# Performance work log

Measured on AMD Instinct MI355X. Metric: run time of the kernel, lower is better.

## Reference

```python
import jax, jax.numpy as jnp
from jax import lax
import numpy as np

DIM = 384
HEADS = 8
SR = 2
B, D0, D1, D2 = 4, 16, 16, 16
N = 1 + D0 * D1 * D2


def setup_inputs() -> dict:
    key = jax.random.key(0)
    ks = jax.random.split(key, 8)
    s = 0.02
    return {
        "x": jax.random.normal(ks[0], (B, N, DIM), dtype=jnp.float32),
        "q_w": jax.random.normal(ks[1], (DIM, DIM), dtype=jnp.float32) * s,
        "kv_w": jax.random.normal(ks[2], (2 * DIM, DIM), dtype=jnp.float32) * s,
        "proj_w": jax.random.normal(ks[3], (DIM, DIM), dtype=jnp.float32) * s,
        "proj_b": jnp.zeros((DIM,), dtype=jnp.float32),
        "sr_w": jax.random.normal(ks[4], (DIM, 1, SR, SR, SR), dtype=jnp.float32) * s,  # depthwise (groups=dim)
        "sr_b": jnp.zeros((DIM,), dtype=jnp.float32),
        "ln_g": jnp.ones((DIM,), dtype=jnp.float32),
        "ln_b": jnp.zeros((DIM,), dtype=jnp.float32),
        "d0": D0, "d1": D1, "d2": D2,
    }


def reference(x, q_w, kv_w, proj_w, proj_b, sr_w, sr_b, ln_g, ln_b, d0, d1, d2):
    B_, N_, C = x.shape
    hd = C // HEADS
    scale = hd ** -0.5

    # q projection -> [B, H, N, hd]
    q = (x @ q_w.T).reshape(B_, N_, HEADS, hd).transpose(0, 2, 1, 3)

    # spatial reduction of patch tokens (keep CLS token)
    x_ = x[:, 1:].transpose(0, 2, 1).reshape(B_, C, d0, d1, d2)
    x_ = lax.conv_general_dilated(
        x_, sr_w, window_strides=(SR, SR, SR), padding="VALID",
        dimension_numbers=("NCDHW", "OIDHW", "NCDHW"), feature_group_count=C,
    ) + sr_b[None, :, None, None, None]
    x_ = x_.reshape(B_, C, -1).transpose(0, 2, 1)           # [B, M-1, C]
    x_ = jnp.concatenate([x[:, 0:1], x_], axis=1)            # [B, M, C]

    # LayerNorm (eps=1e-5)
    mu = jnp.mean(x_, axis=-1, keepdims=True)
    var = jnp.var(x_, axis=-1, keepdims=True)
    x_ = (x_ - mu) / jnp.sqrt(var + 1e-5) * ln_g + ln_b

    M = x_.shape[1]
    kv = (x_ @ kv_w.T).reshape(B_, M, 2, HEADS, hd).transpose(2, 0, 3, 1, 4)
    k, v = kv[0], kv[1]                                      # [B, H, M, hd]

    attn = jax.nn.softmax(jnp.einsum("bhnd,bhmd->bhnm", q, k) * scale, axis=-1)
    out = jnp.einsum("bhnm,bhmd->bhnd", attn, v)
    out = out.transpose(0, 2, 1, 3).reshape(B_, N_, C)
    return out @ proj_w.T + proj_b
```

## Files before the change

kernel.cpp:

```cpp
#include <hip/hip_runtime.h>

typedef unsigned short u16;
typedef unsigned int u32;
typedef __bf16 bf16x8 __attribute__((ext_vector_type(8)));
typedef float f32x4 __attribute__((ext_vector_type(4)));

#define NTOK 4097
#define MTOK 513
#define MPAD 544
#define KPAD 640
#define NPAD_Q 4224
#define ROWS_X 16512

__device__ __forceinline__ u16 f2bf(float f) {
  u32 u = __builtin_bit_cast(u32, f);
  u = u + 0x7FFFu + ((u >> 16) & 1u);
  return (u16)(u >> 16);
}
__device__ __forceinline__ u16 f2bf_fast(float f) {
  u32 u = __builtin_bit_cast(u32, f);
  return (u16)((u + 0x8000u) >> 16);
}

__device__ __forceinline__ float fexp2(float x) {
#if __has_builtin(__builtin_amdgcn_exp2f)
  return __builtin_amdgcn_exp2f(x);
#else
  float r;
  asm("v_exp_f32 %0, %1" : "=v"(r) : "v"(x));
  return r;
#endif
}

__device__ __forceinline__ void gld16(const u16* g, u16* l) {
  __builtin_amdgcn_global_load_lds((const __attribute__((address_space(1))) u32*)g,
                                   (__attribute__((address_space(3))) u32*)l, 16, 0, 0);
}

__device__ __forceinline__ void remap387(int bx, int& row, int& colg) {
  if (bx < 384) {
    int chunk = bx / 24, rem = bx % 24;
    colg = rem >> 3;
    row = chunk * 8 + (rem & 7);
  } else {
    row = 128;
    colg = bx - 384;
  }
}

#define NQW  147456
#define NKVW 294912
#define NPW  147456
#define GQW  (NQW / 8)
#define GKVW (NKVW / 8)
#define GPW  (NPW / 8)
#define GW   (GQW + GKVW + GPW)
#define SRLN_BLOCKS (4 * MTOK)
#define CAST_BLOCKS 192

__global__ void pre_kernel(const float* __restrict__ x, const float* __restrict__ qw,
                           const float* __restrict__ kvw, const float* __restrict__ pw,
                           const float* __restrict__ srw, const float* __restrict__ srb,
                           const float* __restrict__ lng, const float* __restrict__ lnb,
                           u16* __restrict__ qwb, u16* __restrict__ kvwb, u16* __restrict__ pwb,
                           u16* __restrict__ xln) {
  if (blockIdx.x < SRLN_BLOCKS) {
    int c = threadIdx.x;
    int bm = blockIdx.x;
    int b = bm / MTOK, m = bm - b * MTOK;
    float v;
    if (m == 0) {
      v = x[(b * NTOK) * 384 + c];
    } else {
      int mo = m - 1;
      int oz = mo >> 6, oy = (mo >> 3) & 7, ox = mo & 7;
      float acc = srb[c];
#pragma unroll
      for (int dz = 0; dz < 2; dz++)
#pragma unroll
        for (int dy = 0; dy < 2; dy++)
#pragma unroll
          for (int dx = 0; dx < 2; dx++) {
            int tok = 1 + ((2 * oz + dz) * 256 + (2 * oy + dy) * 16 + (2 * ox + dx));
            acc += x[(b * NTOK + tok) * 384 + c] * srw[c * 8 + dz * 4 + dy * 2 + dx];
          }
      v = acc;
    }
    float s1 = v, s2 = v * v;
#pragma unroll
    for (int msk = 32; msk >= 1; msk >>= 1) {
      s1 += __shfl_xor(s1, msk);
      s2 += __shfl_xor(s2, msk);
    }
    __shared__ float r1[6], r2[6];
    int w = threadIdx.x >> 6, lane = threadIdx.x & 63;
    if (lane == 0) { r1[w] = s1; r2[w] = s2; }
    __syncthreads();
    float S1 = 0.f, S2 = 0.f;
#pragma unroll
    for (int i = 0; i < 6; i++) { S1 += r1[i]; S2 += r2[i]; }
    float mu = S1 * (1.0f / 384.0f);
    float var = S2 * (1.0f / 384.0f) - mu * mu;
    float y = (v - mu) * rsqrtf(var + 1e-5f) * lng[c] + lnb[c];
    xln[(b * MPAD + m) * 384 + c] = f2bf(y);
  } else {
    int idx = (blockIdx.x - SRLN_BLOCKS) * blockDim.x + threadIdx.x;
    int stride = (gridDim.x - SRLN_BLOCKS) * blockDim.x;
    for (int g = idx; g < GW; g += stride) {
      const float* s;
      u16* d;
      int off;
      if (g < GQW) { s = qw; d = qwb; off = g * 8; }
      else if (g < GQW + GKVW) { s = kvw; d = kvwb; off = (g - GQW) * 8; }
      else { s = pw; d = pwb; off = (g - GQW - GKVW) * 8; }
      float4 v0 = *(const float4*)(s + off);
      float4 v1 = *(const float4*)(s + off + 4);
      uint4 o;
      u16* p = (u16*)&o;
      p[0] = f2bf(v0.x); p[1] = f2bf(v0.y); p[2] = f2bf(v0.z); p[3] = f2bf(v0.w);
      p[4] = f2bf(v1.x); p[5] = f2bf(v1.y); p[6] = f2bf(v1.z); p[7] = f2bf(v1.w);
      *(uint4*)(d + off) = o;
    }
  }
}

__device__ __forceinline__ void gemm_core(u16* aLds, u16* bLds,
                                          const u16* __restrict__ A, const u16* __restrict__ W,
                                          int mode, size_t rbase, int c0,
                                          u16* __restrict__ o1, u16* __restrict__ o2,
                                          float* __restrict__ of, const float* __restrict__ bias) {
  int tid = threadIdx.x, w = tid >> 6, lane = tid & 63, q4 = lane >> 4, c16 = lane & 15;
  int wr = w >> 1, wc = w & 1;
  int x7 = c16 & 7;

  auto stageAB = [&](int kc, int buf) {
#pragma unroll
    for (int i = 0; i < 4; i++) {
      int s = (w * 4 + i) * 64 + lane;
      int row = s >> 3, chp = s & 7;
      int ch = chp ^ (row & 7);
      gld16(A + (rbase + row) * 384 + kc * 64 + ch * 8, &aLds[buf * 8192 + (w * 4 + i) * 512]);
    }
#pragma unroll
    for (int i = 0; i < 4; i++) {
      int s = (w * 4 + i) * 64 + lane;
      int row = s >> 3, chp = s & 7;
      int ch = chp ^ (row & 7);
      gld16(W + (size_t)(c0 + row) * 384 + kc * 64 + ch * 8, &bLds[buf * 8192 + (w * 4 + i) * 512]);
    }
  };
  stageAB(0, 0);
  __syncthreads();

  f32x4 acc[4][4];
#pragma unroll
  for (int mt = 0; mt < 4; mt++)
#pragma unroll
    for (int nt = 0; nt < 4; nt++) acc[mt][nt] = (f32x4){0, 0, 0, 0};

  for (int c = 0; c < 6; c++) {
    int cb = c & 1, nb = cb ^ 1;
    if (c < 5) stageAB(c + 1, nb);
#pragma unroll
    for (int ks = 0; ks < 2; ks++) {
      bf16x8 af[4], bf[4];
#pragma unroll
      for (int mt = 0; mt < 4; mt++)
        af[mt] = *(const bf16x8*)(&aLds[cb * 8192 + (wr * 64 + mt * 16 + c16) * 64 + ((ks * 4 + q4) ^ x7) * 8]);
#pragma unroll
      for (int nt = 0; nt < 4; nt++)
        bf[nt] = *(const bf16x8*)(&bLds[cb * 8192 + (wc * 64 + nt * 16 + c16) * 64 + ((ks * 4 + q4) ^ x7) * 8]);
#pragma unroll
      for (int mt = 0; mt < 4; mt++)
#pragma unroll
        for (int nt = 0; nt < 4; nt++)
          acc[mt][nt] = __builtin_amdgcn_mfma_f32_16x16x32_bf16(af[mt], bf[nt], acc[mt][nt], 0, 0, 0);
    }
    __syncthreads();
  }

#pragma unroll
  for (int mt = 0; mt < 4; mt++)
#pragma unroll
    for (int nt = 0; nt < 4; nt++) {
      int col = c0 + wc * 64 + nt * 16 + c16;
#pragma unroll
      for (int r = 0; r < 4; r++) {
        int R = (int)rbase + wr * 64 + mt * 16 + q4 * 4 + r;
        float val = acc[mt][nt][r];
        if (mode == 1) {
          int b = R / MPAD;
          int m = R - b * MPAD;
          if (col < 384) {
            int h = col / 48, d = col - h * 48;
            o1[((size_t)(b * 8 + h) * KPAD + m) * 64 + d] = f2bf(val);
          } else {
            int c2 = col - 384;
            int h = c2 / 48, d = c2 - h * 48;
            o2[((size_t)(b * 8 + h) * 48 + d) * KPAD + m] = f2bf(val);
          }
        } else {
          if (R < 4 * NTOK) of[(size_t)R * 384 + col] = val + bias[col];
        }
      }
    }
}

__device__ __forceinline__ void gemm_core_f32A(u16* aLds, u16* bLds,
                                               const float* __restrict__ X, const u16* __restrict__ W,
                                               size_t rbase, int c0, u16* __restrict__ o1) {
  int tid = threadIdx.x, w = tid >> 6, lane = tid & 63, q4 = lane >> 4, c16 = lane & 15;
  int wr = w >> 1, wc = w & 1;
  int x7 = c16 & 7;

  float4 ra[2][2];
  auto loadA2 = [&](int kc, int half) {
#pragma unroll
    for (int i = 0; i < 2; i++) {
      int idx2 = half * 2 + i;
      int s = (w * 4 + idx2) * 64 + lane;
      int row = s >> 3, chp = s & 7;
      int ch = chp ^ (row & 7);
      int ar = (int)rbase + row;
      if (ar > 16387) ar = 16387;
      const float* pa = X + (size_t)ar * 384 + kc * 64 + ch * 8;
      ra[i][0] = *(const float4*)pa;
      ra[i][1] = *(const float4*)(pa + 4);
    }
  };
  auto writeA2 = [&](int buf, int half) {
#pragma unroll
    for (int i = 0; i < 2; i++) {
      int idx2 = half * 2 + i;
      uint4 oa;
      u16* p = (u16*)&oa;
      p[0] = f2bf(ra[i][0].x); p[1] = f2bf(ra[i][0].y);
      p[2] = f2bf(ra[i][0].z); p[3] = f2bf(ra[i][0].w);
      p[4] = f2bf(ra[i][1].x); p[5] = f2bf(ra[i][1].y);
      p[6] = f2bf(ra[i][1].z); p[7] = f2bf(ra[i][1].w);
      *(uint4*)(&aLds[buf * 8192 + (w * 4 + idx2) * 512 + lane * 8]) = oa;
    }
  };
  auto stageB = [&](int kc, int buf) {
#pragma unroll
    for (int i = 0; i < 4; i++) {
      int s = (w * 4 + i) * 64 + lane;
      int row = s >> 3, chp = s & 7;
      int ch = chp ^ (row & 7);
      gld16(W + (size_t)(c0 + row) * 384 + kc * 64 + ch * 8, &bLds[buf * 8192 + (w * 4 + i) * 512]);
    }
  };

  loadA2(0, 0);
  stageB(0, 0);
  writeA2(0, 0);
  loadA2(0, 1);
  writeA2(0, 1);
  __syncthreads();

  f32x4 acc[4][4];
#pragma unroll
  for (int mt = 0; mt < 4; mt++)
#pragma unroll
    for (int nt = 0; nt < 4; nt++) acc[mt][nt] = (f32x4){0, 0, 0, 0};

  for (int c = 0; c < 6; c++) {
    int cb = c & 1, nb = cb ^ 1;
    if (c < 5) { loadA2(c + 1, 0); stageB(c + 1, nb); }
    {
      bf16x8 af[4], bf[4];
#pragma unroll
      for (int mt = 0; mt < 4; mt++)
        af[mt] = *(const bf16x8*)(&aLds[cb * 8192 + (wr * 64 + mt * 16 + c16) * 64 + ((0 + q4) ^ x7) * 8]);
#pragma unroll
      for (int nt = 0; nt < 4; nt++)
        bf[nt] = *(const bf16x8*)(&bLds[cb * 8192 + (wc * 64 + nt * 16 + c16) * 64 + ((0 + q4) ^ x7) * 8]);
#pragma unroll
      for (int mt = 0; mt < 4; mt++)
#pragma unroll
        for (int nt = 0; nt < 4; nt++)
          acc[mt][nt] = __builtin_amdgcn_mfma_f32_16x16x32_bf16(af[mt], bf[nt], acc[mt][nt], 0, 0, 0);
    }
    if (c < 5) { writeA2(nb, 0); loadA2(c + 1, 1); }
    {
      bf16x8 af[4], bf[4];
#pragma unroll
      for (int mt = 0; mt < 4; mt++)
        af[mt] = *(const bf16x8*)(&aLds[cb * 8192 + (wr * 64 + mt * 16 + c16) * 64 + ((4 + q4) ^ x7) * 8]);
#pragma unroll
      for (int nt = 0; nt < 4; nt++)
        bf[nt] = *(const bf16x8*)(&bLds[cb * 8192 + (wc * 64 + nt * 16 + c16) * 64 + ((4 + q4) ^ x7) * 8]);
#pragma unroll
      for (int mt = 0; mt < 4; mt++)
#pragma unroll
        for (int nt = 0; nt < 4; nt++)
          acc[mt][nt] = __builtin_amdgcn_mfma_f32_16x16x32_bf16(af[mt], bf[nt], acc[mt][nt], 0, 0, 0);
    }
    if (c < 5) writeA2(nb, 1);
    __syncthreads();
  }

#pragma unroll
  for (int mt = 0; mt < 4; mt++)
#pragma unroll
    for (int nt = 0; nt < 4; nt++) {
      int col = c0 + wc * 64 + nt * 16 + c16;
#pragma unroll
      for (int r = 0; r < 4; r++) {
        int R = (int)rbase + wr * 64 + mt * 16 + q4 * 4 + r;
        int b = R / NTOK;
        if (b >= 4) continue;
        int n = R - b * NTOK;
        int h = col / 48, d = col - h * 48;
        o1[((size_t)(b * 8 + h) * NPAD_Q + n) * 64 + d] =
            f2bf(acc[mt][nt][r] * (0.14433756729740643f * 1.4426950408889634f));
      }
    }
}

__global__ __launch_bounds__(256) void gemm_qkv(const float* __restrict__ x, const u16* __restrict__ qwb,
                                                const u16* __restrict__ xlnb, const u16* __restrict__ kvwb,
                                                u16* __restrict__ qb, u16* __restrict__ kb2,
                                                u16* __restrict__ vtb) {
  __shared__ __align__(16) u16 aLds[2 * 128 * 64];
  __shared__ __align__(16) u16 bLds[2 * 128 * 64];
  int bx = blockIdx.x;
  if (bx < 387) {
    int row, colg;
    remap387(bx, row, colg);
    gemm_core_f32A(aLds, bLds, x, qwb, (size_t)row * 128, colg * 128, qb);
  } else {
    int i = bx - 387;
    gemm_core(aLds, bLds, xlnb, kvwb, 1, (size_t)(i % 17) * 128, (i / 17) * 128,
              kb2, vtb, nullptr, nullptr);
  }
}

__global__ __launch_bounds__(256) void gemm_out(const u16* __restrict__ A, const u16* __restrict__ W,
                                                float* __restrict__ of, const float* __restrict__ bias) {
  __shared__ __align__(16) u16 aLds[2 * 128 * 64];
  __shared__ __align__(16) u16 bLds[2 * 128 * 64];
  int row, colg;
  remap387(blockIdx.x, row, colg);
  gemm_core(aLds, bLds, A, W, 2, (size_t)row * 128, colg * 128,
            nullptr, nullptr, of, bias);
}

__global__ __launch_bounds__(256, 4) void attn_kernel(const u16* __restrict__ qb,
                                                      const u16* __restrict__ kb,
                                                      const u16* __restrict__ vt,
                                                      u16* __restrict__ outb) {
  __shared__ __align__(16) u16 klds[2][64][64];
  __shared__ __align__(16) u16 vlds[2][48][64];
  __shared__ __align__(16) u16 plds[4][16][76];
  int tid = threadIdx.x, w = tid >> 6, lane = tid & 63, q4 = lane >> 4, c16 = lane & 15;
  int bh = blockIdx.x;
  int n0 = blockIdx.y * 128 + w * 32;
  int r7 = c16 & 7;

  const uint4* qp = (const uint4*)(qb + ((size_t)bh * NPAD_Q + n0 + c16) * 64);
  bf16x8 aq[2][2];
#pragma unroll
  for (int rg = 0; rg < 2; rg++) {
    aq[rg][0] = __builtin_bit_cast(bf16x8, qp[rg * 128 + q4]);
    aq[rg][1] = __builtin_bit_cast(bf16x8, qp[rg * 128 + 4 + q4]);
  }

  const u16* kbase = kb + (size_t)bh * KPAD * 64;
  const u16* vbase = vt + (size_t)bh * 48 * KPAD;

  auto stage = [&](int cn, int buf) {
#pragma unroll
    for (int i = 0; i < 2; i++) {
      int s = (w * 2 + i) * 64 + lane;
      int row = s >> 3, chp = s & 7;
      int ch = chp ^ (row & 7);
      gld16(kbase + (size_t)(cn * 64 + row) * 64 + ch * 8, &klds[buf][(w * 2 + i) * 8][0]);
    }
#pragma unroll
    for (int i = 0; i < 2; i++) {
      int blk = w * 2 + i;
      if (blk < 6) {
        int s = blk * 64 + lane;
        int row = s >> 3, chp = s & 7;
        int ch = chp ^ (row & 7);
        gld16(vbase + (size_t)row * KPAD + cn * 64 + ch * 8, &vlds[buf][blk * 8][0]);
      }
    }
  };

  stage(0, 0);
  __syncthreads();

  f32x4 o[2][3];
  float lsum[2][4];
#pragma unroll
  for (int rg = 0; rg < 2; rg++) {
#pragma unroll
    for (int nt = 0; nt < 3; nt++) o[rg][nt] = (f32x4){0, 0, 0, 0};
#pragma unroll
    for (int r = 0; r < 4; r++) lsum[rg][r] = 0.f;
  }

  for (int c = 0; c < 8; c++) {
    int cb = c & 1, nb = cb ^ 1;
    stage(c + 1, nb);

    f32x4 s[2][4];
#pragma unroll
    for (int rg = 0; rg < 2; rg++)
#pragma unroll
      for (int t = 0; t < 4; t++) s[rg][t] = (f32x4){0, 0, 0, 0};
    __builtin_amdgcn_s_setprio(1);
#pragma unroll
    for (int t = 0; t < 4; t++) {
      const u16* krow = &klds[cb][t * 16 + c16][0];
      bf16x8 k0 = *(const bf16x8*)(krow + (q4 ^ r7) * 8);
      bf16x8 k1 = *(const bf16x8*)(krow + ((q4 ^ r7) ^ 4) * 8);
#pragma unroll
      for (int rg = 0; rg < 2; rg++) {
        s[rg][t] = __builtin_amdgcn_mfma_f32_16x16x32_bf16(aq[rg][0], k0, s[rg][t], 0, 0, 0);
        s[rg][t] = __builtin_amdgcn_mfma_f32_16x16x32_bf16(aq[rg][1], k1, s[rg][t], 0, 0, 0);
      }
    }
    __builtin_amdgcn_s_setprio(0);
#pragma unroll
    for (int rg = 0; rg < 2; rg++)
#pragma unroll
      for (int t = 0; t < 4; t++)
#pragma unroll
        for (int r = 0; r < 4; r++) {
          float e = fexp2(s[rg][t][r]);
          s[rg][t][r] = e;
          lsum[rg][r] += e;
        }
    bf16x8 afrag[2][2];
#pragma unroll
    for (int rg = 0; rg < 2; rg++) {
#pragma unroll
      for (int t = 0; t < 4; t++)
#pragma unroll
        for (int r = 0; r < 4; r++) plds[w][q4 * 4 + r][t * 16 + c16] = f2bf_fast(s[rg][t][r]);
#pragma unroll
      for (int kl = 0; kl < 2; kl++)
        afrag[rg][kl] = *(const bf16x8*)(&plds[w][c16][kl * 32 + q4 * 8]);
    }
    __builtin_amdgcn_s_setprio(1);
#pragma unroll
    for (int kl = 0; kl < 2; kl++)
#pragma unroll
      for (int nt = 0; nt < 3; nt++) {
        const u16* vrow = &vlds[cb][nt * 16 + c16][0];
        bf16x8 bv = *(const bf16x8*)(vrow + ((kl * 4 + q4) ^ r7) * 8);
#pragma unroll
        for (int rg = 0; rg < 2; rg++)
          o[rg][nt] = __builtin_amdgcn_mfma_f32_16x16x32_bf16(afrag[rg][kl], bv, o[rg][nt], 0, 0, 0);
      }
    __builtin_amdgcn_s_setprio(0);
    __syncthreads();
  }

  {
    f32x4 s4[2] = {{0, 0, 0, 0}, {0, 0, 0, 0}};
    const u16* krow = &klds[0][c16][0];
    bf16x8 k0 = *(const bf16x8*)(krow + (q4 ^ r7) * 8);
    bf16x8 k1 = *(const bf16x8*)(krow + ((q4 ^ r7) ^ 4) * 8);
#pragma unroll
    for (int rg = 0; rg < 2; rg++) {
      s4[rg] = __builtin_amdgcn_mfma_f32_16x16x32_bf16(aq[rg][0], k0, s4[rg], 0, 0, 0);
      s4[rg] = __builtin_amdgcn_mfma_f32_16x16x32_bf16(aq[rg][1], k1, s4[rg], 0, 0, 0);
    }
    bf16x8 afrag[2];
#pragma unroll
    for (int rg = 0; rg < 2; rg++) {
#pragma unroll
      for (int r = 0; r < 4; r++) {
        float e = (c16 == 0) ? fexp2(s4[rg][r]) : 0.f;
        lsum[rg][r] += e;
        plds[w][q4 * 4 + r][c16] = f2bf_fast(e);
        plds[w][q4 * 4 + r][16 + c16] = 0;
      }
      afrag[rg] = *(const bf16x8*)(&plds[w][c16][q4 * 8]);
    }
#pragma unroll
    for (int nt = 0; nt < 3; nt++) {
      const u16* vrow = &vlds[0][nt * 16 + c16][0];
      bf16x8 bv = *(const bf16x8*)(vrow + (q4 ^ r7) * 8);
#pragma unroll
      for (int rg = 0; rg < 2; rg++)
        o[rg][nt] = __builtin_amdgcn_mfma_f32_16x16x32_bf16(afrag[rg], bv, o[rg][nt], 0, 0, 0);
    }
  }

  int b = bh >> 3, h = bh & 7;
#pragma unroll
  for (int rg = 0; rg < 2; rg++) {
    float inv[4];
#pragma unroll
    for (int r = 0; r < 4; r++) {
      float l = lsum[rg][r];
      l += __shfl_xor(l, 1);
      l += __shfl_xor(l, 2);
      l += __shfl_xor(l, 4);
      l += __shfl_xor(l, 8);
      inv[r] = 1.0f / l;
    }
#pragma unroll
    for (int nt = 0; nt < 3; nt++)
#pragma unroll
      for (int r = 0; r < 4; r++) {
        int n = n0 + rg * 16 + q4 * 4 + r;
        if (n < NTOK) outb[((size_t)(b * NTOK + n)) * 384 + h * 48 + nt * 16 + c16] = f2bf(o[rg][nt][r] * inv[r]);
      }
  }
}

extern "C" void kernel_launch(void* const* d_in, const int* in_sizes, int n_in,
                              void* d_out, int out_size, void* d_ws, size_t ws_size,
                              hipStream_t stream) {
  const float* x = (const float*)d_in[0];
  const float* q_w = (const float*)d_in[1];
  const float* kv_w = (const float*)d_in[2];
  const float* proj_w = (const float*)d_in[3];
  const float* proj_b = (const float*)d_in[4];
  const float* sr_w = (const float*)d_in[5];
  const float* sr_b = (const float*)d_in[6];
  const float* ln_g = (const float*)d_in[7];
  const float* ln_b = (const float*)d_in[8];
  float* out = (float*)d_out;

  u16* ws = (u16*)d_ws;
  u16* x_b = ws;
  u16* qw_b = x_b + (size_t)ROWS_X * 384;
  u16* kvw_b = qw_b + 147456;
  u16* pw_b = kvw_b + 294912;
  u16* q_b = pw_b + 147456;
  u16* xln_b = q_b + (size_t)32 * NPAD_Q * 64;
  u16* k_b = xln_b + (size_t)4 * MPAD * 384;
  u16* vt_b = k_b + (size_t)32 * KPAD * 64;
  u16* attn_b = x_b;


  pre_kernel<<<SRLN_BLOCKS + CAST_BLOCKS, 384, 0, stream>>>(x, q_w, kv_w, proj_w, sr_w, sr_b,
                                                            ln_g, ln_b, qw_b, kvw_b, pw_b, xln_b);
  gemm_qkv<<<489, 256, 0, stream>>>(x, qw_b, xln_b, kvw_b, q_b, k_b, vt_b);
  attn_kernel<<<dim3(32, 33), 256, 0, stream>>>(q_b, k_b, vt_b, attn_b);
  gemm_out<<<387, 256, 0, stream>>>(attn_b, pw_b, out, proj_b);
}
```

Measured before the change: 166.5 us.

## Fuse kv and proj weight fp32-to-bf16 casts into GEMM B-tile staging

The pre-kernel now casts only q_w to bf16. The kv and proj GEMMs read fp32 weights directly, convert them in registers and write single-buffered LDS tiles, while A stays double-buffered through async global-to-LDS loads. The q GEMM's fp32 A path is simplified to a single LDS buffer, shrinking shared memory to 48KB with launch bounds of 3 blocks per CU. This removes the separate weight cast pass and its extra global traffic, at the cost of loading fp32 weights again from every block and adding a sync per k-step.

```diff
diff --git a/kernel.cpp b/kernel.cpp
--- a/kernel.cpp
+++ b/kernel.cpp
@@ -49,21 +49,14 @@
 }
 
 #define NQW  147456
-#define NKVW 294912
-#define NPW  147456
 #define GQW  (NQW / 8)
-#define GKVW (NKVW / 8)
-#define GPW  (NPW / 8)
-#define GW   (GQW + GKVW + GPW)
 #define SRLN_BLOCKS (4 * MTOK)
-#define CAST_BLOCKS 192
+#define CAST_BLOCKS 48
 
 __global__ void pre_kernel(const float* __restrict__ x, const float* __restrict__ qw,
-                           const float* __restrict__ kvw, const float* __restrict__ pw,
                            const float* __restrict__ srw, const float* __restrict__ srb,
                            const float* __restrict__ lng, const float* __restrict__ lnb,
-                           u16* __restrict__ qwb, u16* __restrict__ kvwb, u16* __restrict__ pwb,
-                           u16* __restrict__ xln) {
+                           u16* __restrict__ qwb, u16* __restrict__ xln) {
   if (blockIdx.x < SRLN_BLOCKS) {
     int c = threadIdx.x;
     int bm = blockIdx.x;
@@ -104,36 +97,148 @@
     float y = (v - mu) * rsqrtf(var + 1e-5f) * lng[c] + lnb[c];
     xln[(b * MPAD + m) * 384 + c] = f2bf(y);
   } else {
-    int idx = (blockIdx.x - SRLN_BLOCKS) * blockDim.x + threadIdx.x;
-    int stride = (gridDim.x - SRLN_BLOCKS) * blockDim.x;
-    for (int g = idx; g < GW; g += stride) {
-      const float* s;
-      u16* d;
-      int off;
-      if (g < GQW) { s = qw; d = qwb; off = g * 8; }
-      else if (g < GQW + GKVW) { s = kvw; d = kvwb; off = (g - GQW) * 8; }
-      else { s = pw; d = pwb; off = (g - GQW - GKVW) * 8; }
-      float4 v0 = *(const float4*)(s + off);
-      float4 v1 = *(const float4*)(s + off + 4);
-      uint4 o;
-      u16* p = (u16*)&o;
-      p[0] = f2bf(v0.x); p[1] = f2bf(v0.y); p[2] = f2bf(v0.z); p[3] = f2bf(v0.w);
-      p[4] = f2bf(v1.x); p[5] = f2bf(v1.y); p[6] = f2bf(v1.z); p[7] = f2bf(v1.w);
-      *(uint4*)(d + off) = o;
-    }
-  }
-}
-
-__device__ __forceinline__ void gemm_core(u16* aLds, u16* bLds,
-                                          const u16* __restrict__ A, const u16* __restrict__ W,
-                                          int mode, size_t rbase, int c0,
-                                          u16* __restrict__ o1, u16* __restrict__ o2,
-                                          float* __restrict__ of, const float* __restrict__ bias) {
+    int g = (blockIdx.x - SRLN_BLOCKS) * blockDim.x + threadIdx.x;
+    int off = g * 8;
+    float4 v0 = *(const float4*)(qw + off);
+    float4 v1 = *(const float4*)(qw + off + 4);
+    uint4 o;
+    u16* p = (u16*)&o;
+    p[0] = f2bf(v0.x); p[1] = f2bf(v0.y); p[2] = f2bf(v0.z); p[3] = f2bf(v0.w);
+    p[4] = f2bf(v1.x); p[5] = f2bf(v1.y); p[6] = f2bf(v1.z); p[7] = f2bf(v1.w);
+    *(uint4*)(qwb + off) = o;
+  }
+}
+
+__device__ __forceinline__ void gemm_core_sa(u16* aLds, u16* bLds,
+                                             const float* __restrict__ X, const u16* __restrict__ W,
+                                             size_t rbase, int c0, u16* __restrict__ o1) {
   int tid = threadIdx.x, w = tid >> 6, lane = tid & 63, q4 = lane >> 4, c16 = lane & 15;
   int wr = w >> 1, wc = w & 1;
   int x7 = c16 & 7;
 
-  auto stageAB = [&](int kc, int buf) {
+  float4 ra[4][2];
+  auto loadA = [&](int kc) {
+#pragma unroll
+    for (int i = 0; i < 4; i++) {
+      int s = (w * 4 + i) * 64 + lane;
+      int row = s >> 3, chp = s & 7;
+      int ch = chp ^ (row & 7);
+      int ar = (int)rbase + row;
+      if (ar > 16387) ar = 16387;
+      const float* pa = X + (size_t)ar * 384 + kc * 64 + ch * 8;
+      ra[i][0] = *(const float4*)pa;
+      ra[i][1] = *(const float4*)(pa + 4);
+    }
+  };
+  auto writeA = [&]() {
+#pragma unroll
+    for (int i = 0; i < 4; i++) {
+      uint4 oa;
+      u16* p = (u16*)&oa;
+      p[0] = f2bf(ra[i][0].x); p[1] = f2bf(ra[i][0].y);
+      p[2] = f2bf(ra[i][0].z); p[3] = f2bf(ra[i][0].w);
+      p[4] = f2bf(ra[i][1].x); p[5] = f2bf(ra[i][1].y);
+      p[6] = f2bf(ra[i][1].z); p[7] = f2bf(ra[i][1].w);
+      *(uint4*)(&aLds[(w * 4 + i) * 512 + lane * 8]) = oa;
+    }
+  };
+  auto stageB = [&](int kc, int buf) {
+#pragma unroll
+    for (int i = 0; i < 4; i++) {
+      int s = (w * 4 + i) * 64 + lane;
+      int row = s >> 3, chp = s & 7;
+      int ch = chp ^ (row & 7);
+      gld16(W + (size_t)(c0 + row) * 384 + kc * 64 + ch * 8, &bLds[buf * 8192 + (w * 4 + i) * 512]);
+    }
+  };
+
+  loadA(0);
+  stageB(0, 0);
+
+  f32x4 acc[4][4];
+#pragma unroll
+  for (int mt = 0; mt < 4; mt++)
+#pragma unroll
+    for (int nt = 0; nt < 4; nt++) acc[mt][nt] = (f32x4){0, 0, 0, 0};
+
+  for (int c = 0; c < 6; c++) {
+    int cb = c & 1, nb = cb ^ 1;
+    writeA();
+    __syncthreads();
+    if (c < 5) {
+      stageB(c + 1, nb);
+      loadA(c + 1);
+    }
+#pragma unroll
+    for (int ks = 0; ks < 2; ks++) {
+      bf16x8 af[4], bf[4];
+#pragma unroll
+      for (int mt = 0; mt < 4; mt++)
+        af[mt] = *(const bf16x8*)(&aLds[(wr * 64 + mt * 16 + c16) * 64 + ((ks * 4 + q4) ^ x7) * 8]);
+#pragma unroll
+      for (int nt = 0; nt < 4; nt++)
+        bf[nt] = *(const bf16x8*)(&bLds[cb * 8192 + (wc * 64 + nt * 16 + c16) * 64 + ((ks * 4 + q4) ^ x7) * 8]);
+#pragma unroll
+      for (int mt = 0; mt < 4; mt++)
+#pragma unroll
+        for (int nt = 0; nt < 4; nt++)
+          acc[mt][nt] = __builtin_amdgcn_mfma_f32_16x16x32_bf16(af[mt], bf[nt], acc[mt][nt], 0, 0, 0);
+    }
+    __syncthreads();
+  }
+
+#pragma unroll
+  for (int mt = 0; mt < 4; mt++)
+#pragma unroll
+    for (int nt = 0; nt < 4; nt++) {
+      int col = c0 + wc * 64 + nt * 16 + c16;
+#pragma unroll
+      for (int r = 0; r < 4; r++) {
+        int R = (int)rbase + wr * 64 + mt * 16 + q4 * 4 + r;
+        int b = R / NTOK;
+        if (b >= 4) continue;
+        int n = R - b * NTOK;
+        int h = col / 48, d = col - h * 48;
+        o1[((size_t)(b * 8 + h) * NPAD_Q + n) * 64 + d] =
+            f2bf(acc[mt][nt][r] * (0.14433756729740643f * 1.4426950408889634f));
+      }
+    }
+}
+
+__device__ __forceinline__ void gemm_core_sb(u16* aLds, u16* bLds,
+                                             const u16* __restrict__ A, const float* __restrict__ WF,
+                                             int mode, size_t rbase, int c0,
+                                             u16* __restrict__ o1, u16* __restrict__ o2,
+                                             float* __restrict__ of, const float* __restrict__ bias) {
+  int tid = threadIdx.x, w = tid >> 6, lane = tid & 63, q4 = lane >> 4, c16 = lane & 15;
+  int wr = w >> 1, wc = w & 1;
+  int x7 = c16 & 7;
+
+  float4 rb[4][2];
+  auto loadB = [&](int kc) {
+#pragma unroll
+    for (int i = 0; i < 4; i++) {
+      int s = (w * 4 + i) * 64 + lane;
+      int row = s >> 3, chp = s & 7;
+      int ch = chp ^ (row & 7);
+      const float* pb = WF + (size_t)(c0 + row) * 384 + kc * 64 + ch * 8;
+      rb[i][0] = *(const float4*)pb;
+      rb[i][1] = *(const float4*)(pb + 4);
+    }
+  };
+  auto writeB = [&]() {
+#pragma unroll
+    for (int i = 0; i < 4; i++) {
+      uint4 ob;
+      u16* p = (u16*)&ob;
+      p[0] = f2bf(rb[i][0].x); p[1] = f2bf(rb[i][0].y);
+      p[2] = f2bf(rb[i][0].z); p[3] = f2bf(rb[i][0].w);
+      p[4] = f2bf(rb[i][1].x); p[5] = f2bf(rb[i][1].y);
+      p[6] = f2bf(rb[i][1].z); p[7] = f2bf(rb[i][1].w);
+      *(uint4*)(&bLds[(w * 4 + i) * 512 + lane * 8]) = ob;
+    }
+  };
+  auto stageA = [&](int kc, int buf) {
 #pragma unroll
     for (int i = 0; i < 4; i++) {
       int s = (w * 4 + i) * 64 + lane;
@@ -141,16 +246,10 @@
       int ch = chp ^ (row & 7);
       gld16(A + (rbase + row) * 384 + kc * 64 + ch * 8, &aLds[buf * 8192 + (w * 4 + i) * 512]);
     }
-#pragma unroll
-    for (int i = 0; i < 4; i++) {
-      int s = (w * 4 + i) * 64 + lane;
-      int row = s >> 3, chp = s & 7;
-      int ch = chp ^ (row & 7);
-      gld16(W + (size_t)(c0 + row) * 384 + kc * 64 + ch * 8, &bLds[buf * 8192 + (w * 4 + i) * 512]);
-    }
-  };
-  stageAB(0, 0);
-  __syncthreads();
+  };
+
+  loadB(0);
+  stageA(0, 0);
 
   f32x4 acc[4][4];
 #pragma unroll
@@ -160,7 +259,12 @@
 
   for (int c = 0; c < 6; c++) {
     int cb = c & 1, nb = cb ^ 1;
-    if (c < 5) stageAB(c + 1, nb);
+    writeB();
+    __syncthreads();
+    if (c < 5) {
+      stageA(c + 1, nb);
+      loadB(c + 1);
+    }
 #pragma unroll
     for (int ks = 0; ks < 2; ks++) {
       bf16x8 af[4], bf[4];
@@ -169,7 +273,7 @@
         af[mt] = *(const bf16x8*)(&aLds[cb * 8192 + (wr * 64 + mt * 16 + c16) * 64 + ((ks * 4 + q4) ^ x7) * 8]);
 #pragma unroll
       for (int nt = 0; nt < 4; nt++)
-        bf[nt] = *(const bf16x8*)(&bLds[cb * 8192 + (wc * 64 + nt * 16 + c16) * 64 + ((ks * 4 + q4) ^ x7) * 8]);
+        bf[nt] = *(const bf16x8*)(&bLds[(wc * 64 + nt * 16 + c16) * 64 + ((ks * 4 + q4) ^ x7) * 8]);
 #pragma unroll
       for (int mt = 0; mt < 4; mt++)
 #pragma unroll
@@ -206,144 +310,30 @@
     }
 }
 
-__device__ __forceinline__ void gemm_core_f32A(u16* aLds, u16* bLds,
-                                               const float* __restrict__ X, const u16* __restrict__ W,
-                                               size_t rbase, int c0, u16* __restrict__ o1) {
-  int tid = threadIdx.x, w = tid >> 6, lane = tid & 63, q4 = lane >> 4, c16 = lane & 15;
-  int wr = w >> 1, wc = w & 1;
-  int x7 = c16 & 7;
-
-  float4 ra[2][2];
-  auto loadA2 = [&](int kc, int half) {
-#pragma unroll
-    for (int i = 0; i < 2; i++) {
-      int idx2 = half * 2 + i;
-      int s = (w * 4 + idx2) * 64 + lane;
-      int row = s >> 3, chp = s & 7;
-      int ch = chp ^ (row & 7);
-      int ar = (int)rbase + row;
-      if (ar > 16387) ar = 16387;
-      const float* pa = X + (size_t)ar * 384 + kc * 64 + ch * 8;
-      ra[i][0] = *(const float4*)pa;
-      ra[i][1] = *(const float4*)(pa + 4);
-    }
-  };
-  auto writeA2 = [&](int buf, int half) {
-#pragma unroll
-    for (int i = 0; i < 2; i++) {
-      int idx2 = half * 2 + i;
-      uint4 oa;
-      u16* p = (u16*)&oa;
-      p[0] = f2bf(ra[i][0].x); p[1] = f2bf(ra[i][0].y);
-      p[2] = f2bf(ra[i][0].z); p[3] = f2bf(ra[i][0].w);
-      p[4] = f2bf(ra[i][1].x); p[5] = f2bf(ra[i][1].y);
-      p[6] = f2bf(ra[i][1].z); p[7] = f2bf(ra[i][1].w);
-      *(uint4*)(&aLds[buf * 8192 + (w * 4 + idx2) * 512 + lane * 8]) = oa;
-    }
-  };
-  auto stageB = [&](int kc, int buf) {
-#pragma unroll
-    for (int i = 0; i < 4; i++) {
-      int s = (w * 4 + i) * 64 + lane;
-      int row = s >> 3, chp = s & 7;
-      int ch = chp ^ (row & 7);
-      gld16(W + (size_t)(c0 + row) * 384 + kc * 64 + ch * 8, &bLds[buf * 8192 + (w * 4 + i) * 512]);
-    }
-  };
-
-  loadA2(0, 0);
-  stageB(0, 0);
-  writeA2(0, 0);
-  loadA2(0, 1);
-  writeA2(0, 1);
-  __syncthreads();
-
-  f32x4 acc[4][4];
-#pragma unroll
-  for (int mt = 0; mt < 4; mt++)
-#pragma unroll
-    for (int nt = 0; nt < 4; nt++) acc[mt][nt] = (f32x4){0, 0, 0, 0};
-
-  for (int c = 0; c < 6; c++) {
-    int cb = c & 1, nb = cb ^ 1;
-    if (c < 5) { loadA2(c + 1, 0); stageB(c + 1, nb); }
-    {
-      bf16x8 af[4], bf[4];
-#pragma unroll
-      for (int mt = 0; mt < 4; mt++)
-        af[mt] = *(const bf16x8*)(&aLds[cb * 8192 + (wr * 64 + mt * 16 + c16) * 64 + ((0 + q4) ^ x7) * 8]);
-#pragma unroll
-      for (int nt = 0; nt < 4; nt++)
-        bf[nt] = *(const bf16x8*)(&bLds[cb * 8192 + (wc * 64 + nt * 16 + c16) * 64 + ((0 + q4) ^ x7) * 8]);
-#pragma unroll
-      for (int mt = 0; mt < 4; mt++)
-#pragma unroll
-        for (int nt = 0; nt < 4; nt++)
-          acc[mt][nt] = __builtin_amdgcn_mfma_f32_16x16x32_bf16(af[mt], bf[nt], acc[mt][nt], 0, 0, 0);
-    }
-    if (c < 5) { writeA2(nb, 0); loadA2(c + 1, 1); }
-    {
-      bf16x8 af[4], bf[4];
-#pragma unroll
-      for (int mt = 0; mt < 4; mt++)
-        af[mt] = *(const bf16x8*)(&aLds[cb * 8192 + (wr * 64 + mt * 16 + c16) * 64 + ((4 + q4) ^ x7) * 8]);
-#pragma unroll
-      for (int nt = 0; nt < 4; nt++)
-        bf[nt] = *(const bf16x8*)(&bLds[cb * 8192 + (wc * 64 + nt * 16 + c16) * 64 + ((4 + q4) ^ x7) * 8]);
-#pragma unroll
-      for (int mt = 0; mt < 4; mt++)
-#pragma unroll
-        for (int nt = 0; nt < 4; nt++)
-          acc[mt][nt] = __builtin_amdgcn_mfma_f32_16x16x32_bf16(af[mt], bf[nt], acc[mt][nt], 0, 0, 0);
-    }
-    if (c < 5) writeA2(nb, 1);
-    __syncthreads();
-  }
-
-#pragma unroll
-  for (int mt = 0; mt < 4; mt++)
-#pragma unroll
-    for (int nt = 0; nt < 4; nt++) {
-      int col = c0 + wc * 64 + nt * 16 + c16;
-#pragma unroll
-      for (int r = 0; r < 4; r++) {
-        int R = (int)rbase + wr * 64 + mt * 16 + q4 * 4 + r;
-        int b = R / NTOK;
-        if (b >= 4) continue;
-        int n = R - b * NTOK;
-        int h = col / 48, d = col - h * 48;
-        o1[((size_t)(b * 8 + h) * NPAD_Q + n) * 64 + d] =
-            f2bf(acc[mt][nt][r] * (0.14433756729740643f * 1.4426950408889634f));
-      }
-    }
-}
-
-__global__ __launch_bounds__(256) void gemm_qkv(const float* __restrict__ x, const u16* __restrict__ qwb,
-                                                const u16* __restrict__ xlnb, const u16* __restrict__ kvwb,
-                                                u16* __restrict__ qb, u16* __restrict__ kb2,
-                                                u16* __restrict__ vtb) {
-  __shared__ __align__(16) u16 aLds[2 * 128 * 64];
-  __shared__ __align__(16) u16 bLds[2 * 128 * 64];
+__global__ __launch_bounds__(256, 3) void gemm_qkv(const float* __restrict__ x, const u16* __restrict__ qwb,
+                                                   const u16* __restrict__ xlnb, const float* __restrict__ kvwf,
+                                                   u16* __restrict__ qb, u16* __restrict__ kb2,
+                                                   u16* __restrict__ vtb) {
+  __shared__ __align__(16) u16 smem[24576];
   int bx = blockIdx.x;
   if (bx < 387) {
     int row, colg;
     remap387(bx, row, colg);
-    gemm_core_f32A(aLds, bLds, x, qwb, (size_t)row * 128, colg * 128, qb);
+    gemm_core_sa(smem, smem + 8192, x, qwb, (size_t)row * 128, colg * 128, qb);
   } else {
     int i = bx - 387;
-    gemm_core(aLds, bLds, xlnb, kvwb, 1, (size_t)(i % 17) * 128, (i / 17) * 128,
-              kb2, vtb, nullptr, nullptr);
-  }
-}
-
-__global__ __launch_bounds__(256) void gemm_out(const u16* __restrict__ A, const u16* __restrict__ W,
-                                                float* __restrict__ of, const float* __restrict__ bias) {
-  __shared__ __align__(16) u16 aLds[2 * 128 * 64];
-  __shared__ __align__(16) u16 bLds[2 * 128 * 64];
+    gemm_core_sb(smem, smem + 16384, xlnb, kvwf, 1, (size_t)(i % 17) * 128, (i / 17) * 128,
+                 kb2, vtb, nullptr, nullptr);
+  }
+}
+
+__global__ __launch_bounds__(256, 3) void gemm_out(const u16* __restrict__ A, const float* __restrict__ WF,
+                                                   float* __restrict__ of, const float* __restrict__ bias) {
+  __shared__ __align__(16) u16 smem[24576];
   int row, colg;
   remap387(blockIdx.x, row, colg);
-  gemm_core(aLds, bLds, A, W, 2, (size_t)row * 128, colg * 128,
-            nullptr, nullptr, of, bias);
+  gemm_core_sb(smem, smem + 16384, A, WF, 2, (size_t)row * 128, colg * 128,
+               nullptr, nullptr, of, bias);
 }
 
 __global__ __launch_bounds__(256, 4) void attn_kernel(const u16* __restrict__ qb,
@@ -541,9 +531,9 @@
   u16* attn_b = x_b;
 
 
-  pre_kernel<<<SRLN_BLOCKS + CAST_BLOCKS, 384, 0, stream>>>(x, q_w, kv_w, proj_w, sr_w, sr_b,
-                                                            ln_g, ln_b, qw_b, kvw_b, pw_b, xln_b);
-  gemm_qkv<<<489, 256, 0, stream>>>(x, qw_b, xln_b, kvw_b, q_b, k_b, vt_b);
+  pre_kernel<<<SRLN_BLOCKS + CAST_BLOCKS, 384, 0, stream>>>(x, q_w, sr_w, sr_b,
+                                                            ln_g, ln_b, qw_b, xln_b);
+  gemm_qkv<<<489, 256, 0, stream>>>(x, qw_b, xln_b, kv_w, q_b, k_b, vt_b);
   attn_kernel<<<dim3(32, 33), 256, 0, stream>>>(q_b, k_b, vt_b, attn_b);
-  gemm_out<<<387, 256, 0, stream>>>(attn_b, pw_b, out, proj_b);
-}
+  gemm_out<<<387, 256, 0, stream>>>(attn_b, proj_w, out, proj_b);
+}
```

Result: no change. 169.2 us (+1.7%).
